# Optimization experiments

Hardware: AMD Instinct MI355X
Metric: run time of the kernel (lower is better)

## Reference

```python
import jax, jax.numpy as jnp
import numpy as np

B, S, D, H = 4, 2048, 1024, 16
HD = D // H  # head_dim = 64

def setup_inputs() -> dict:
    key = jax.random.key(0)
    ks = jax.random.split(key, 5)
    scale = 1.0 / np.sqrt(D)
    return {
        "x": jax.random.normal(ks[0], (B, S, D), dtype=jnp.float32),
        "Wqkv": jax.random.normal(ks[1], (D, 3 * D), dtype=jnp.float32) * scale,
        "bqkv": jax.random.normal(ks[2], (3 * D,), dtype=jnp.float32) * 0.01,
        "Wo": jax.random.normal(ks[3], (D, D), dtype=jnp.float32) * scale,
        "bo": jax.random.normal(ks[4], (D,), dtype=jnp.float32) * 0.01,
    }

def reference(x, Wqkv, bqkv, Wo, bo):
    b, s, d = x.shape
    # fused QKV projection: [B,S,3D]
    qkv = jnp.einsum("bsd,de->bse", x, Wqkv) + bqkv
    # [B,S,H,3*HD] -> [B,H,S,3*HD], then chunk into q,k,v per head
    qkv = qkv.reshape(b, s, H, 3 * HD).transpose(0, 2, 1, 3)
    q, k, v = jnp.split(qkv, 3, axis=-1)  # each [B,H,S,HD]
    inv_sqrt_dk = jnp.asarray(1.0 / np.sqrt(HD), dtype=x.dtype)
    scores = jnp.einsum("bhqd,bhkd->bhqk", q, k) * inv_sqrt_dk
    attn = jax.nn.softmax(scores, axis=-1)
    values = jnp.einsum("bhqk,bhkd->bhqd", attn, v)  # [B,H,S,HD]
    # NOTE: source reshapes [B,H,S,HD] -> [B,S,H*HD] WITHOUT permuting back
    # (a quirk of the original code); replicated faithfully.
    values = values.reshape(b, s, d)
    out = jnp.einsum("bsd,de->bse", values, Wo) + bo
    return out
```

## Files before the change

### kernel.cpp

```cpp
#include <hip/hip_runtime.h>
#include <hip/hip_bf16.h>
#include <cstdint>

static constexpr int Bq  = 4;
static constexpr int Sq  = 2048;
static constexpr int Dq  = 1024;
static constexpr int Hq  = 16;
static constexpr int HDq = 64;
static constexpr int ROWS = Bq * Sq;
static constexpr int QKV_N = 3 * Dq;

typedef __bf16 bf16x8 __attribute__((ext_vector_type(8)));
typedef __bf16 bf16x4 __attribute__((ext_vector_type(4)));
typedef __bf16 bf16x2 __attribute__((ext_vector_type(2)));
typedef float  floatx4 __attribute__((ext_vector_type(4)));
typedef float  floatx16 __attribute__((ext_vector_type(16)));
typedef unsigned int uintx4 __attribute__((ext_vector_type(4)));

#define MFMA16(a, b, c) __builtin_amdgcn_mfma_f32_16x16x32_bf16((a), (b), (c), 0, 0, 0)
#define MFMA32(a, b, c) __builtin_amdgcn_mfma_f32_32x32x16_bf16((a), (b), (c), 0, 0, 0)

#define QSCALE 0.18033688011112042f

__device__ __forceinline__ void async16(const void* g, void* l) {
    __builtin_amdgcn_global_load_lds(
        (const __attribute__((address_space(1))) uint32_t*)g,
        (__attribute__((address_space(3))) uint32_t*)l, 16, 0, 0);
}

__global__ __launch_bounds__(256) void cvt4_kernel(const float4* __restrict__ in,
                                                   bf16x4* __restrict__ out, int n4) {
    int i = blockIdx.x * 256 + threadIdx.x;
    if (i < n4) {
        float4 v = in[i];
        bf16x4 o;
        o[0] = (__bf16)v.x; o[1] = (__bf16)v.y; o[2] = (__bf16)v.z; o[3] = (__bf16)v.w;
        out[i] = o;
    }
}

__global__ __launch_bounds__(256) void tcvt_kernel(const float* __restrict__ in,
                                                   __bf16* __restrict__ out, int K, int N) {
    __shared__ float t[32][33];
    int n0 = blockIdx.x * 32, k0 = blockIdx.y * 32;
    int c = threadIdx.x & 31, r0 = threadIdx.x >> 5;
#pragma unroll
    for (int rr = 0; rr < 32; rr += 8)
        t[r0 + rr][c] = in[(size_t)(k0 + r0 + rr) * N + n0 + c];
    __syncthreads();
#pragma unroll
    for (int rr = 0; rr < 32; rr += 8)
        out[(size_t)(n0 + r0 + rr) * K + k0 + c] = (__bf16)t[c][r0 + rr];
}

__global__ __launch_bounds__(512, 2) void gemm_qkv_kernel(const __bf16* __restrict__ A,
                                                          const __bf16* __restrict__ BT,
                                                          const float* __restrict__ bias,
                                                          __bf16* __restrict__ qkvb,
                                                          __bf16* __restrict__ Vt) {
    __shared__ __bf16 lds[2][2][2][128][64];

    const int tid  = threadIdx.x;
    const int lane = tid & 63;
    const int wave = tid >> 6;
    const int wm = wave >> 2;
    const int wn = wave & 3;
    const int l31 = lane & 31;
    const int hi  = lane >> 5;
    const int kx  = l31 & 7;

    const int m0 = blockIdx.y * 256;
    const int n0 = blockIdx.x * 256;

    const int srow = lane >> 3;
    const int ssl  = ((lane & 7) ^ srow) * 8;
    const __bf16* gA = A  + (size_t)(m0 + wave * 16 + srow) * 1024 + ssl;
    const __bf16* gB = BT + (size_t)(n0 + wave * 16 + srow) * 1024 + ssl;

    auto STAGE = [&](int buf, int op, int half, int ktel) {
        const __bf16* g = (op ? gB : gA) + (size_t)half * (128 * 1024) + ktel;
        __bf16* l = &lds[buf][op][half][0][0] + wave * 1024 + lane * 8;
        async16(g, l);
        async16(g + 8 * 1024, l + 512);
    };

    floatx16 acc[4][2] = {};

    STAGE(0, 1, 0, 0);
    STAGE(0, 0, 0, 0);
    STAGE(0, 1, 1, 0);
    STAGE(0, 0, 1, 0);
    STAGE(1, 1, 0, 64);
    STAGE(1, 0, 0, 64);
    asm volatile("s_waitcnt vmcnt(4)" ::: "memory");
    __builtin_amdgcn_sched_barrier(0);
    __builtin_amdgcn_s_barrier();

    const int brow = (wn & 1) * 64;

    for (int t = 0; t < 16; ++t) {
        const int d = t & 1;
        const __bf16* As = &lds[d][0][wm][0][0];
        const __bf16* Bs = &lds[d][1][wn >> 1][0][0];

        bf16x8 af[2][4], bf0[4], bf1[4];

#pragma unroll
        for (int mf = 0; mf < 2; ++mf)
#pragma unroll
            for (int ks = 0; ks < 4; ++ks)
                af[mf][ks] = *(const bf16x8*)(As + (mf * 32 + l31) * 64 + ((ks * 2 + hi) ^ kx) * 8);
#pragma unroll
        for (int ks = 0; ks < 4; ++ks)
            bf0[ks] = *(const bf16x8*)(Bs + (brow + l31) * 64 + ((ks * 2 + hi) ^ kx) * 8);
        if (t + 1 < 16) STAGE(d ^ 1, 1, 1, (t + 1) * 64);
        __builtin_amdgcn_s_barrier();
        __builtin_amdgcn_s_setprio(1);
#pragma unroll
        for (int ks = 0; ks < 4; ++ks) {
            acc[0][0] = MFMA32(af[0][ks], bf0[ks], acc[0][0]);
            acc[1][0] = MFMA32(af[1][ks], bf0[ks], acc[1][0]);
        }
        __builtin_amdgcn_s_setprio(0);
        __builtin_amdgcn_s_barrier();

#pragma unroll
        for (int ks = 0; ks < 4; ++ks)
            bf1[ks] = *(const bf16x8*)(Bs + (brow + 32 + l31) * 64 + ((ks * 2 + hi) ^ kx) * 8);
        if (t + 1 < 16) STAGE(d ^ 1, 0, 1, (t + 1) * 64);
        __builtin_amdgcn_s_barrier();
        __builtin_amdgcn_s_setprio(1);
#pragma unroll
        for (int ks = 0; ks < 4; ++ks) {
            acc[0][1] = MFMA32(af[0][ks], bf1[ks], acc[0][1]);
            acc[1][1] = MFMA32(af[1][ks], bf1[ks], acc[1][1]);
        }
        __builtin_amdgcn_s_setprio(0);
        __builtin_amdgcn_s_barrier();

#pragma unroll
        for (int mf = 0; mf < 2; ++mf)
#pragma unroll
            for (int ks = 0; ks < 4; ++ks)
                af[mf][ks] = *(const bf16x8*)(As + ((2 + mf) * 32 + l31) * 64 + ((ks * 2 + hi) ^ kx) * 8);
        if (t + 2 < 16) STAGE(d, 1, 0, (t + 2) * 64);
        __builtin_amdgcn_s_barrier();
        __builtin_amdgcn_s_setprio(1);
#pragma unroll
        for (int ks = 0; ks < 4; ++ks) {
            acc[2][1] = MFMA32(af[0][ks], bf1[ks], acc[2][1]);
            acc[3][1] = MFMA32(af[1][ks], bf1[ks], acc[3][1]);
        }
        __builtin_amdgcn_s_setprio(0);
        __builtin_amdgcn_s_barrier();

        if (t + 2 < 16) STAGE(d, 0, 0, (t + 2) * 64);
        __builtin_amdgcn_s_barrier();
        __builtin_amdgcn_s_setprio(1);
#pragma unroll
        for (int ks = 0; ks < 4; ++ks) {
            acc[2][0] = MFMA32(af[0][ks], bf0[ks], acc[2][0]);
            acc[3][0] = MFMA32(af[1][ks], bf0[ks], acc[3][0]);
        }
        __builtin_amdgcn_s_setprio(0);
        if (t < 14) {
            asm volatile("s_waitcnt vmcnt(4)" ::: "memory");
        } else {
            asm volatile("s_waitcnt vmcnt(0)" ::: "memory");
        }
        __builtin_amdgcn_sched_barrier(0);
        __builtin_amdgcn_s_barrier();
    }

#pragma unroll
    for (int fn = 0; fn < 2; ++fn) {
        const int cg = n0 + wn * 64 + fn * 32;
        const int cm = cg % 192;
        const float bv = bias[cg + l31];
        if (cm >= 128) {
            const int hh = cg / 192;
            const int dd = cm - 128 + l31;
            const int bb = m0 >> 11;
            const int sb = (m0 + wm * 128) & 2047;
            __bf16* vt = Vt + ((size_t)(bb * Hq + hh) * HDq + dd) * Sq + sb;
#pragma unroll
            for (int fm = 0; fm < 4; ++fm)
#pragma unroll
                for (int g = 0; g < 4; ++g) {
                    bf16x4 vv;
#pragma unroll
                    for (int i = 0; i < 4; ++i) vv[i] = (__bf16)(acc[fm][fn][g * 4 + i] + bv);
                    *(bf16x4*)(vt + fm * 32 + g * 8 + hi * 4) = vv;
                }
        } else {
            const float sc = (cm < 64) ? QSCALE : 1.0f;
#pragma unroll
            for (int fm = 0; fm < 4; ++fm)
#pragma unroll
                for (int r = 0; r < 16; ++r) {
                    int m = m0 + wm * 128 + fm * 32 + (r & 3) + 8 * (r >> 2) + 4 * hi;
                    qkvb[(size_t)m * QKV_N + cg + l31] = (__bf16)((acc[fm][fn][r] + bv) * sc);
                }
        }
    }
}

template <int MODE>
__global__ __launch_bounds__(256) void gemm_bt_kernel(const __bf16* __restrict__ A,
                                                      const __bf16* __restrict__ BT,
                                                      const float* __restrict__ bias,
                                                      void* __restrict__ Cout,
                                                      __bf16* __restrict__ Vt,
                                                      int M, int N, int K) {
    __shared__ __bf16 As[128 * 32];
    __shared__ __bf16 Bs[128 * 32];

    const int t = threadIdx.x;
    const int lane = t & 63;
    const int wave = t >> 6;
    const int wm = wave & 1, wn = wave >> 1;
    const int l15 = lane & 15;
    const int kg = (lane >> 4) * 8;

    const int m0 = blockIdx.y * 128;
    const int n0 = blockIdx.x * 128;

    const int srow = t >> 2;
    const int scol = (t & 3) * 8;
    const __bf16* ag = A  + (size_t)(m0 + srow) * K + scol;
    const __bf16* bg = BT + (size_t)(n0 + srow) * K + scol;
    __bf16* al = As + t * 8;
    __bf16* bl = Bs + t * 8;

    floatx4 acc[4][4] = {};

    for (int k0 = 0; k0 < K; k0 += 32) {
        __syncthreads();
        async16(ag + k0,                    al);
        async16(ag + (size_t)64 * K + k0,   al + 2048);
        async16(bg + k0,                    bl);
        async16(bg + (size_t)64 * K + k0,   bl + 2048);
        __syncthreads();

        bf16x8 af[4], bfr[4];
#pragma unroll
        for (int mi = 0; mi < 4; ++mi)
            af[mi] = *(const bf16x8*)(As + (wm * 64 + mi * 16 + l15) * 32 + kg);
#pragma unroll
        for (int ni = 0; ni < 4; ++ni)
            bfr[ni] = *(const bf16x8*)(Bs + (wn * 64 + ni * 16 + l15) * 32 + kg);
#pragma unroll
        for (int mi = 0; mi < 4; ++mi)
#pragma unroll
            for (int ni = 0; ni < 4; ++ni)
                acc[mi][ni] = MFMA16(af[mi], bfr[ni], acc[mi][ni]);
    }

    const int r0 = (lane >> 4) * 4;
    const int wn0 = n0 + wn * 64;

#pragma unroll
    for (int ni = 0; ni < 4; ++ni) {
        int col = wn0 + ni * 16 + l15;
        float bv = bias[col];
#pragma unroll
        for (int mi = 0; mi < 4; ++mi) {
#pragma unroll
            for (int i = 0; i < 4; ++i) {
                int row = m0 + wm * 64 + mi * 16 + r0 + i;
                float v = acc[mi][ni][i] + bv;
                size_t off = (size_t)row * N + col;
                ((float*)Cout)[off] = v;
            }
        }
    }
}

__global__ __launch_bounds__(256, 2) void attn_kernel(const __bf16* __restrict__ qkv,
                                                      const __bf16* __restrict__ Vt,
                                                      __bf16* __restrict__ v2) {
    const int bh = blockIdx.x;
    const int b = bh >> 4, h = bh & 15;
    const int q0 = blockIdx.y * 256;
    const int tid  = threadIdx.x;
    const int lane = tid & 63;
    const int wave = tid >> 6;
    const int l31  = lane & 31;
    const int hi   = lane >> 5;
    const int kx   = l31 & 7;
    const size_t rs = QKV_N;
    const __bf16* base  = qkv + (size_t)b * Sq * rs + (size_t)h * (3 * HDq);
    const __bf16* vbase = Vt + (size_t)bh * HDq * Sq;

    __shared__ alignas(16) __bf16 Ks[2][64][64];
    __shared__ alignas(16) __bf16 Vs[2][64][64];

    bf16x8 qb[2][4];
#pragma unroll
    for (int qg = 0; qg < 2; ++qg) {
        const __bf16* qr = base + (size_t)(q0 + wave * 64 + qg * 32 + l31) * rs + hi * 8;
#pragma unroll
        for (int st = 0; st < 4; ++st) qb[qg][st] = *(const bf16x8*)(qr + st * 16);
    }

    const int rA = wave * 8 + (lane >> 3);
    const int rB = rA + 32;
    const int sw = ((lane & 7) ^ (rA & 7)) * 8;
    const __bf16* gK0 = base + HDq + (size_t)rA * rs + sw;
    const __bf16* gK1 = base + HDq + (size_t)rB * rs + sw;
    const __bf16* gV0 = vbase + (size_t)rA * Sq + sw;
    const __bf16* gV1 = vbase + (size_t)rB * Sq + sw;
    const int loff0 = wave * 512 + lane * 8;
    const int loff1 = (4 + wave) * 512 + lane * 8;

    auto STAGE = [&](int bufi, int kt) {
        const size_t ko = (size_t)kt * rs;
        async16(gK0 + ko, &Ks[bufi][0][0] + loff0);
        async16(gK1 + ko, &Ks[bufi][0][0] + loff1);
        async16(gV0 + kt, &Vs[bufi][0][0] + loff0);
        async16(gV1 + kt, &Vs[bufi][0][0] + loff1);
    };

    auto softmax_pb = [&](const floatx16& c, float& la, bf16x8* pb) {
        unsigned int W[8];
        float s0 = 0.f, s1 = 0.f;
#pragma unroll
        for (int m = 0; m < 8; ++m) {
            float e0 = __builtin_amdgcn_exp2f(c[2 * m]);
            float e1 = __builtin_amdgcn_exp2f(c[2 * m + 1]);
            s0 += e0; s1 += e1;
            union { bf16x2 v; unsigned int u; } pk;
            pk.v[0] = (__bf16)e0; pk.v[1] = (__bf16)e1;
            W[m] = pk.u;
        }
        la += s0 + s1;
#pragma unroll
        for (int ks = 0; ks < 2; ++ks) {
            auto r0 = __builtin_amdgcn_permlane32_swap(W[ks * 4 + 0], W[ks * 4 + 2], false, false);
            auto r1 = __builtin_amdgcn_permlane32_swap(W[ks * 4 + 1], W[ks * 4 + 3], false, false);
            uintx4 bb; bb[0] = r0[0]; bb[1] = r1[0]; bb[2] = r0[1]; bb[3] = r1[1];
            pb[ks] = __builtin_bit_cast(bf16x8, bb);
        }
    };

    floatx16 o[2][2] = {};
    float la0 = 0.f, la1 = 0.f;

    STAGE(0, 0);
    __syncthreads();

    int cur = 0;
    for (int kt = 0; kt < Sq; kt += 64, cur ^= 1) {
        if (kt + 64 < Sq) STAGE(cur ^ 1, kt + 64);

#pragma unroll
        for (int half = 0; half < 2; ++half) {
            const int key = half * 32 + l31;

            floatx16 c0 = {}, c1 = {};
#pragma unroll
            for (int st = 0; st < 4; ++st) {
                bf16x8 a = *(const bf16x8*)(&Ks[cur][key][((st * 2 + hi) ^ kx) * 8]);
                c0 = MFMA32(a, qb[0][st], c0);
                c1 = MFMA32(a, qb[1][st], c1);
            }

            bf16x8 pb0[2], pb1[2];
            softmax_pb(c0, la0, pb0);
            softmax_pb(c1, la1, pb1);

#pragma unroll
            for (int ks = 0; ks < 2; ++ks) {
                const int kslot = half * 4 + ks * 2 + hi;
                bf16x8 va0 = *(const bf16x8*)(&Vs[cur][l31][(kslot ^ kx) * 8]);
                bf16x8 va1 = *(const bf16x8*)(&Vs[cur][32 + l31][(kslot ^ kx) * 8]);
                o[0][0] = MFMA32(va0, pb0[ks], o[0][0]);
                o[0][1] = MFMA32(va1, pb0[ks], o[0][1]);
                o[1][0] = MFMA32(va0, pb1[ks], o[1][0]);
                o[1][1] = MFMA32(va1, pb1[ks], o[1][1]);
            }
        }
        __syncthreads();
    }

#pragma unroll
    for (int qg = 0; qg < 2; ++qg) {
        float lsum = qg ? la1 : la0;
        float l = lsum + __shfl_xor(lsum, 32);
        float rinv = 1.0f / l;
        const int q = q0 + wave * 64 + qg * 32 + l31;
        size_t row = (size_t)b * Sq + h * 128 + (q >> 4);
        __bf16* vrow = v2 + row * Dq + (size_t)(q & 15) * 64;
#pragma unroll
        for (int gg = 0; gg < 4; ++gg) {
            bf16x4 ov;
#pragma unroll
            for (int i = 0; i < 4; ++i) ov[i] = (__bf16)(o[qg][0][gg * 4 + i] * rinv);
            *(bf16x4*)(vrow + gg * 8 + hi * 4) = ov;
#pragma unroll
            for (int i = 0; i < 4; ++i) ov[i] = (__bf16)(o[qg][1][gg * 4 + i] * rinv);
            *(bf16x4*)(vrow + 32 + gg * 8 + hi * 4) = ov;
        }
    }
}

extern "C" void kernel_launch(void* const* d_in, const int* in_sizes, int n_in,
                              void* d_out, int out_size, void* d_ws, size_t ws_size,
                              hipStream_t stream) {
    const float* x    = (const float*)d_in[0];
    const float* Wqkv = (const float*)d_in[1];
    const float* bqkv = (const float*)d_in[2];
    const float* Wo   = (const float*)d_in[3];
    const float* bo   = (const float*)d_in[4];
    float* out = (float*)d_out;

    __bf16* xb    = (__bf16*)d_ws;
    __bf16* WqkvT = xb    + (size_t)ROWS * Dq;
    __bf16* WoT   = WqkvT + (size_t)QKV_N * Dq;
    __bf16* qkvb  = WoT   + (size_t)Dq * Dq;
    __bf16* Vt    = qkvb  + (size_t)ROWS * QKV_N;
    __bf16* v2    = xb;

    const int nx4 = ROWS * Dq / 4;
    cvt4_kernel<<<(nx4 + 255) / 256, 256, 0, stream>>>((const float4*)x, (bf16x4*)xb, nx4);
    tcvt_kernel<<<dim3(QKV_N / 32, Dq / 32), 256, 0, stream>>>(Wqkv, WqkvT, Dq, QKV_N);
    tcvt_kernel<<<dim3(Dq / 32, Dq / 32), 256, 0, stream>>>(Wo, WoT, Dq, Dq);

    gemm_qkv_kernel<<<dim3(QKV_N / 256, ROWS / 256), 512, 0, stream>>>(
        xb, WqkvT, bqkv, qkvb, Vt);

    attn_kernel<<<dim3(Bq * Hq, Sq / 256), 256, 0, stream>>>(qkvb, Vt, v2);

    gemm_bt_kernel<1><<<dim3(Dq / 128, ROWS / 128), 256, 0, stream>>>(
        v2, WoT, bo, (void*)out, nullptr, ROWS, Dq, Dq);
}
```

Baseline: 282.5 us.

## Split attention over the key dimension with a separate combine kernel

```diff
diff --git a/kernel.cpp b/kernel.cpp
--- a/kernel.cpp
+++ b/kernel.cpp
@@ -205,13 +205,11 @@
     }
 }
 
-template <int MODE>
-__global__ __launch_bounds__(256) void gemm_bt_kernel(const __bf16* __restrict__ A,
-                                                      const __bf16* __restrict__ BT,
-                                                      const float* __restrict__ bias,
-                                                      void* __restrict__ Cout,
-                                                      __bf16* __restrict__ Vt,
-                                                      int M, int N, int K) {
+__global__ __launch_bounds__(256) void gemm_out_kernel(const __bf16* __restrict__ A,
+                                                       const __bf16* __restrict__ BT,
+                                                       const float* __restrict__ bias,
+                                                       float* __restrict__ Cout,
+                                                       int M, int N, int K) {
     __shared__ __bf16 As[128 * 32];
     __shared__ __bf16 Bs[128 * 32];
 
@@ -268,18 +266,20 @@
 #pragma unroll
             for (int i = 0; i < 4; ++i) {
                 int row = m0 + wm * 64 + mi * 16 + r0 + i;
-                float v = acc[mi][ni][i] + bv;
-                size_t off = (size_t)row * N + col;
-                ((float*)Cout)[off] = v;
+                Cout[(size_t)row * N + col] = acc[mi][ni][i] + bv;
             }
         }
     }
 }
 
-__global__ __launch_bounds__(256, 2) void attn_kernel(const __bf16* __restrict__ qkv,
+template <int NS>
+__global__ __launch_bounds__(256, 4) void attn_kernel(const __bf16* __restrict__ qkv,
                                                       const __bf16* __restrict__ Vt,
-                                                      __bf16* __restrict__ v2) {
-    const int bh = blockIdx.x;
+                                                      __bf16* __restrict__ v2,
+                                                      float* __restrict__ Opart,
+                                                      float* __restrict__ Lpart) {
+    const int bh = blockIdx.x / NS;
+    const int sp = (NS > 1) ? (blockIdx.x % NS) : 0;
     const int b = bh >> 4, h = bh & 15;
     const int q0 = blockIdx.y * 256;
     const int tid  = threadIdx.x;
@@ -346,12 +346,15 @@
     floatx16 o[2][2] = {};
     float la0 = 0.f, la1 = 0.f;
 
-    STAGE(0, 0);
+    const int kbeg = sp * (Sq / NS);
+    const int kend = kbeg + Sq / NS;
+
+    STAGE(0, kbeg);
     __syncthreads();
 
     int cur = 0;
-    for (int kt = 0; kt < Sq; kt += 64, cur ^= 1) {
-        if (kt + 64 < Sq) STAGE(cur ^ 1, kt + 64);
+    for (int kt = kbeg; kt < kend; kt += 64, cur ^= 1) {
+        if (kt + 64 < kend) STAGE(cur ^ 1, kt + 64);
 
 #pragma unroll
         for (int half = 0; half < 2; ++half) {
@@ -387,21 +390,59 @@
     for (int qg = 0; qg < 2; ++qg) {
         float lsum = qg ? la1 : la0;
         float l = lsum + __shfl_xor(lsum, 32);
-        float rinv = 1.0f / l;
         const int q = q0 + wave * 64 + qg * 32 + l31;
-        size_t row = (size_t)b * Sq + h * 128 + (q >> 4);
-        __bf16* vrow = v2 + row * Dq + (size_t)(q & 15) * 64;
-#pragma unroll
-        for (int gg = 0; gg < 4; ++gg) {
-            bf16x4 ov;
-#pragma unroll
-            for (int i = 0; i < 4; ++i) ov[i] = (__bf16)(o[qg][0][gg * 4 + i] * rinv);
-            *(bf16x4*)(vrow + gg * 8 + hi * 4) = ov;
-#pragma unroll
-            for (int i = 0; i < 4; ++i) ov[i] = (__bf16)(o[qg][1][gg * 4 + i] * rinv);
-            *(bf16x4*)(vrow + 32 + gg * 8 + hi * 4) = ov;
-        }
-    }
+
+        if (NS == 1) {
+            float rinv = 1.0f / l;
+            size_t row = (size_t)b * Sq + h * 128 + (q >> 4);
+            __bf16* vrow = v2 + row * Dq + (size_t)(q & 15) * 64;
+#pragma unroll
+            for (int gg = 0; gg < 4; ++gg) {
+                bf16x4 ov;
+#pragma unroll
+                for (int i = 0; i < 4; ++i) ov[i] = (__bf16)(o[qg][0][gg * 4 + i] * rinv);
+                *(bf16x4*)(vrow + gg * 8 + hi * 4) = ov;
+#pragma unroll
+                for (int i = 0; i < 4; ++i) ov[i] = (__bf16)(o[qg][1][gg * 4 + i] * rinv);
+                *(bf16x4*)(vrow + 32 + gg * 8 + hi * 4) = ov;
+            }
+        } else {
+            const size_t ql = (size_t)bh * Sq + q;
+            if (hi == 0) Lpart[(size_t)sp * (64 * Sq) + ql] = l;
+            float* orow = Opart + ((size_t)sp * (64 * Sq) + ql) * HDq;
+#pragma unroll
+            for (int gg = 0; gg < 4; ++gg) {
+                float4 f0, f1;
+                f0.x = o[qg][0][gg * 4 + 0]; f0.y = o[qg][0][gg * 4 + 1];
+                f0.z = o[qg][0][gg * 4 + 2]; f0.w = o[qg][0][gg * 4 + 3];
+                f1.x = o[qg][1][gg * 4 + 0]; f1.y = o[qg][1][gg * 4 + 1];
+                f1.z = o[qg][1][gg * 4 + 2]; f1.w = o[qg][1][gg * 4 + 3];
+                *(float4*)(orow + gg * 8 + hi * 4)      = f0;
+                *(float4*)(orow + 32 + gg * 8 + hi * 4) = f1;
+            }
+        }
+    }
+}
+
+__global__ __launch_bounds__(256) void combine_kernel(const float4* __restrict__ O,
+                                                      const float* __restrict__ L,
+                                                      __bf16* __restrict__ v2) {
+    const int idx = blockIdx.x * 256 + threadIdx.x;
+    const int d4 = idx & 15;
+    const int ql = idx >> 4;
+    float4 a = O[idx];
+    float4 c = O[2097152 + idx];
+    float rinv = 1.0f / (L[ql] + L[131072 + ql]);
+    const int bh = ql >> 11, q = ql & 2047;
+    const int b = bh >> 4, h = bh & 15;
+    __bf16* dst = v2 + ((size_t)(b * Sq + h * 128 + (q >> 4))) * Dq
+                     + (size_t)(q & 15) * 64 + d4 * 4;
+    bf16x4 o;
+    o[0] = (__bf16)((a.x + c.x) * rinv);
+    o[1] = (__bf16)((a.y + c.y) * rinv);
+    o[2] = (__bf16)((a.z + c.z) * rinv);
+    o[3] = (__bf16)((a.w + c.w) * rinv);
+    *(bf16x4*)dst = o;
 }
 
 extern "C" void kernel_launch(void* const* d_in, const int* in_sizes, int n_in,
@@ -420,6 +461,11 @@
     __bf16* qkvb  = WoT   + (size_t)Dq * Dq;
     __bf16* Vt    = qkvb  + (size_t)ROWS * QKV_N;
     __bf16* v2    = xb;
+    float*  Opart = (float*)(Vt + (size_t)Bq * Hq * HDq * Sq);
+    float*  Lpart = Opart + (size_t)2 * 131072 * 64;
+
+    const size_t need = (size_t)((char*)(Lpart + 2 * 131072) - (char*)d_ws);
+    const bool use_split = ws_size >= need;
 
     const int nx4 = ROWS * Dq / 4;
     cvt4_kernel<<<(nx4 + 255) / 256, 256, 0, stream>>>((const float4*)x, (bf16x4*)xb, nx4);
@@ -429,8 +475,16 @@
     gemm_qkv_kernel<<<dim3(QKV_N / 256, ROWS / 256), 512, 0, stream>>>(
         xb, WqkvT, bqkv, qkvb, Vt);
 
-    attn_kernel<<<dim3(Bq * Hq, Sq / 256), 256, 0, stream>>>(qkvb, Vt, v2);
-
-    gemm_bt_kernel<1><<<dim3(Dq / 128, ROWS / 128), 256, 0, stream>>>(
-        v2, WoT, bo, (void*)out, nullptr, ROWS, Dq, Dq);
-}
+    if (use_split) {
+        attn_kernel<2><<<dim3(Bq * Hq * 2, Sq / 256), 256, 0, stream>>>(
+            qkvb, Vt, nullptr, Opart, Lpart);
+        combine_kernel<<<2097152 / 256, 256, 0, stream>>>(
+            (const float4*)Opart, Lpart, v2);
+    } else {
+        attn_kernel<1><<<dim3(Bq * Hq, Sq / 256), 256, 0, stream>>>(
+            qkvb, Vt, v2, nullptr, nullptr);
+    }
+
+    gemm_out_kernel<<<dim3(Dq / 128, ROWS / 128), 256, 0, stream>>>(
+        v2, WoT, bo, out, ROWS, Dq, Dq);
+}
```

Measured after the change: 709.5 us. 151% more time.

## Fuse prep kernels and restructure attention loop to interleave softmax with MFMA

Applied to the files above, without the earlier changes.

```diff
diff --git a/kernel.cpp b/kernel.cpp
--- a/kernel.cpp
+++ b/kernel.cpp
@@ -28,22 +28,28 @@
         (__attribute__((address_space(3))) uint32_t*)l, 16, 0, 0);
 }
 
-__global__ __launch_bounds__(256) void cvt4_kernel(const float4* __restrict__ in,
-                                                   bf16x4* __restrict__ out, int n4) {
-    int i = blockIdx.x * 256 + threadIdx.x;
-    if (i < n4) {
-        float4 v = in[i];
+__global__ __launch_bounds__(256) void prep_kernel(const float4* __restrict__ x4,
+                                                   bf16x4* __restrict__ xb4,
+                                                   const float* __restrict__ Wqkv,
+                                                   __bf16* __restrict__ WqkvT,
+                                                   const float* __restrict__ Wo,
+                                                   __bf16* __restrict__ WoT) {
+    __shared__ float t[32][33];
+    const int bx = blockIdx.x;
+    if (bx < 8192) {
+        int i = bx * 256 + threadIdx.x;
+        float4 v = x4[i];
         bf16x4 o;
         o[0] = (__bf16)v.x; o[1] = (__bf16)v.y; o[2] = (__bf16)v.z; o[3] = (__bf16)v.w;
-        out[i] = o;
-    }
-}
-
-__global__ __launch_bounds__(256) void tcvt_kernel(const float* __restrict__ in,
-                                                   __bf16* __restrict__ out, int K, int N) {
-    __shared__ float t[32][33];
-    int n0 = blockIdx.x * 32, k0 = blockIdx.y * 32;
-    int c = threadIdx.x & 31, r0 = threadIdx.x >> 5;
+        xb4[i] = o;
+        return;
+    }
+    const float* in; __bf16* out; int K, N, bid;
+    if (bx < 8192 + 3072) { bid = bx - 8192;  in = Wqkv; out = WqkvT; K = Dq; N = QKV_N; }
+    else                  { bid = bx - 11264; in = Wo;   out = WoT;   K = Dq; N = Dq; }
+    const int nt = N / 32;
+    const int n0 = (bid % nt) * 32, k0 = (bid / nt) * 32;
+    const int c = threadIdx.x & 31, r0 = threadIdx.x >> 5;
 #pragma unroll
     for (int rr = 0; rr < 32; rr += 8)
         t[r0 + rr][c] = in[(size_t)(k0 + r0 + rr) * N + n0 + c];
@@ -205,13 +211,11 @@
     }
 }
 
-template <int MODE>
-__global__ __launch_bounds__(256) void gemm_bt_kernel(const __bf16* __restrict__ A,
-                                                      const __bf16* __restrict__ BT,
-                                                      const float* __restrict__ bias,
-                                                      void* __restrict__ Cout,
-                                                      __bf16* __restrict__ Vt,
-                                                      int M, int N, int K) {
+__global__ __launch_bounds__(256) void gemm_out_kernel(const __bf16* __restrict__ A,
+                                                       const __bf16* __restrict__ BT,
+                                                       const float* __restrict__ bias,
+                                                       float* __restrict__ Cout,
+                                                       int M, int N, int K) {
     __shared__ __bf16 As[128 * 32];
     __shared__ __bf16 Bs[128 * 32];
 
@@ -268,9 +272,7 @@
 #pragma unroll
             for (int i = 0; i < 4; ++i) {
                 int row = m0 + wm * 64 + mi * 16 + r0 + i;
-                float v = acc[mi][ni][i] + bv;
-                size_t off = (size_t)row * N + col;
-                ((float*)Cout)[off] = v;
+                Cout[(size_t)row * N + col] = acc[mi][ni][i] + bv;
             }
         }
     }
@@ -353,33 +355,53 @@
     for (int kt = 0; kt < Sq; kt += 64, cur ^= 1) {
         if (kt + 64 < Sq) STAGE(cur ^ 1, kt + 64);
 
-#pragma unroll
-        for (int half = 0; half < 2; ++half) {
-            const int key = half * 32 + l31;
-
-            floatx16 c0 = {}, c1 = {};
-#pragma unroll
-            for (int st = 0; st < 4; ++st) {
-                bf16x8 a = *(const bf16x8*)(&Ks[cur][key][((st * 2 + hi) ^ kx) * 8]);
-                c0 = MFMA32(a, qb[0][st], c0);
-                c1 = MFMA32(a, qb[1][st], c1);
-            }
-
-            bf16x8 pb0[2], pb1[2];
-            softmax_pb(c0, la0, pb0);
-            softmax_pb(c1, la1, pb1);
-
-#pragma unroll
-            for (int ks = 0; ks < 2; ++ks) {
-                const int kslot = half * 4 + ks * 2 + hi;
-                bf16x8 va0 = *(const bf16x8*)(&Vs[cur][l31][(kslot ^ kx) * 8]);
-                bf16x8 va1 = *(const bf16x8*)(&Vs[cur][32 + l31][(kslot ^ kx) * 8]);
-                o[0][0] = MFMA32(va0, pb0[ks], o[0][0]);
-                o[0][1] = MFMA32(va1, pb0[ks], o[0][1]);
-                o[1][0] = MFMA32(va0, pb1[ks], o[1][0]);
-                o[1][1] = MFMA32(va1, pb1[ks], o[1][1]);
-            }
-        }
+        bf16x8 ka0[4], ka1[4];
+#pragma unroll
+        for (int st = 0; st < 4; ++st) {
+            ka0[st] = *(const bf16x8*)(&Ks[cur][l31][((st * 2 + hi) ^ kx) * 8]);
+            ka1[st] = *(const bf16x8*)(&Ks[cur][32 + l31][((st * 2 + hi) ^ kx) * 8]);
+        }
+        floatx16 c00 = {}, c01 = {}, c10 = {}, c11 = {};
+        __builtin_amdgcn_s_setprio(1);
+#pragma unroll
+        for (int st = 0; st < 4; ++st) {
+            c00 = MFMA32(ka0[st], qb[0][st], c00);
+            c10 = MFMA32(ka1[st], qb[0][st], c10);
+            c01 = MFMA32(ka0[st], qb[1][st], c01);
+            c11 = MFMA32(ka1[st], qb[1][st], c11);
+        }
+        __builtin_amdgcn_s_setprio(0);
+
+        bf16x8 pb00[2], pb01[2], pb10[2], pb11[2];
+        softmax_pb(c00, la0, pb00);
+        softmax_pb(c01, la1, pb01);
+        __builtin_amdgcn_s_setprio(1);
+#pragma unroll
+        for (int ks = 0; ks < 2; ++ks) {
+            const int kslot = ks * 2 + hi;
+            bf16x8 va0 = *(const bf16x8*)(&Vs[cur][l31][(kslot ^ kx) * 8]);
+            bf16x8 va1 = *(const bf16x8*)(&Vs[cur][32 + l31][(kslot ^ kx) * 8]);
+            o[0][0] = MFMA32(va0, pb00[ks], o[0][0]);
+            o[0][1] = MFMA32(va1, pb00[ks], o[0][1]);
+            o[1][0] = MFMA32(va0, pb01[ks], o[1][0]);
+            o[1][1] = MFMA32(va1, pb01[ks], o[1][1]);
+        }
+        __builtin_amdgcn_s_setprio(0);
+        softmax_pb(c10, la0, pb10);
+        softmax_pb(c11, la1, pb11);
+        __builtin_amdgcn_s_setprio(1);
+#pragma unroll
+        for (int ks = 0; ks < 2; ++ks) {
+            const int kslot = 4 + ks * 2 + hi;
+            bf16x8 va0 = *(const bf16x8*)(&Vs[cur][l31][(kslot ^ kx) * 8]);
+            bf16x8 va1 = *(const bf16x8*)(&Vs[cur][32 + l31][(kslot ^ kx) * 8]);
+            o[0][0] = MFMA32(va0, pb10[ks], o[0][0]);
+            o[0][1] = MFMA32(va1, pb10[ks], o[0][1]);
+            o[1][0] = MFMA32(va0, pb11[ks], o[1][0]);
+            o[1][1] = MFMA32(va1, pb11[ks], o[1][1]);
+        }
+        __builtin_amdgcn_s_setprio(0);
+
         __syncthreads();
     }
 
@@ -421,16 +443,14 @@
     __bf16* Vt    = qkvb  + (size_t)ROWS * QKV_N;
     __bf16* v2    = xb;
 
-    const int nx4 = ROWS * Dq / 4;
-    cvt4_kernel<<<(nx4 + 255) / 256, 256, 0, stream>>>((const float4*)x, (bf16x4*)xb, nx4);
-    tcvt_kernel<<<dim3(QKV_N / 32, Dq / 32), 256, 0, stream>>>(Wqkv, WqkvT, Dq, QKV_N);
-    tcvt_kernel<<<dim3(Dq / 32, Dq / 32), 256, 0, stream>>>(Wo, WoT, Dq, Dq);
+    prep_kernel<<<12288, 256, 0, stream>>>((const float4*)x, (bf16x4*)xb,
+                                           Wqkv, WqkvT, Wo, WoT);
 
     gemm_qkv_kernel<<<dim3(QKV_N / 256, ROWS / 256), 512, 0, stream>>>(
         xb, WqkvT, bqkv, qkvb, Vt);
 
     attn_kernel<<<dim3(Bq * Hq, Sq / 256), 256, 0, stream>>>(qkvb, Vt, v2);
 
-    gemm_bt_kernel<1><<<dim3(Dq / 128, ROWS / 128), 256, 0, stream>>>(
-        v2, WoT, bo, (void*)out, nullptr, ROWS, Dq, Dq);
-}
+    gemm_out_kernel<<<dim3(Dq / 128, ROWS / 128), 256, 0, stream>>>(
+        v2, WoT, bo, out, ROWS, Dq, Dq);
+}
```

Measured after the change: 269.6 us. 4.6% less time.
